# Kernel tuning notes

Measured on AMD Instinct MI355X. Metric: run time of the kernel, lower is better.

The kernel has to match this reference:

```python
import jax, jax.numpy as jnp
import numpy as np

B, S, IN, H, NH, PF, L = 8, 1024, 256, 1024, 16, 4096, 6
HD = H // NH
EPS = 1e-5


def _layernorm(x, g, b):
    m = jnp.mean(x, axis=-1, keepdims=True)
    v = jnp.mean((x - m) ** 2, axis=-1, keepdims=True)
    return (x - m) * jax.lax.rsqrt(v + EPS) * g + b


def setup_inputs() -> dict:
    key = jax.random.key(0)
    ks = iter(jax.random.split(key, 40))
    sd = 0.02
    inp = {
        "input_x": jax.random.normal(next(ks), (B, S, IN), jnp.float32),
        "emb_W": jax.random.normal(next(ks), (IN, H), jnp.float32) * sd,
        "emb_b": jnp.zeros((H,), jnp.float32),
        "pos_tab": jax.random.normal(next(ks), (S, H), jnp.float32) * sd,
        "Wq": jax.random.normal(next(ks), (L, H, H), jnp.float32) * sd,
        "bq": jnp.zeros((L, H), jnp.float32),
        "Wk": jax.random.normal(next(ks), (L, H, H), jnp.float32) * sd,
        "bk": jnp.zeros((L, H), jnp.float32),
        "Wv": jax.random.normal(next(ks), (L, H, H), jnp.float32) * sd,
        "bv": jnp.zeros((L, H), jnp.float32),
        "Wo": jax.random.normal(next(ks), (L, H, H), jnp.float32) * sd,
        "bo": jnp.zeros((L, H), jnp.float32),
        "ln1_g": jnp.ones((L, H), jnp.float32),
        "ln1_b": jnp.zeros((L, H), jnp.float32),
        "W1": jax.random.normal(next(ks), (L, H, PF), jnp.float32) * sd,
        "b1": jnp.zeros((L, PF), jnp.float32),
        "W2": jax.random.normal(next(ks), (L, PF, H), jnp.float32) * sd,
        "b2": jnp.zeros((L, H), jnp.float32),
        "ln2_g": jnp.ones((L, H), jnp.float32),
        "ln2_b": jnp.zeros((L, H), jnp.float32),
    }
    return inp


def _encoder(input_x, emb_W, emb_b, pos_tab, Wq, bq, Wk, bk, Wv, bv, Wo, bo,
             ln1_g, ln1_b, W1, b1, W2, b2, ln2_g, ln2_b):
    scale = jnp.sqrt(jnp.float32(H))  # module scales by sqrt(hidden_size)
    x = (input_x @ emb_W + emb_b) * scale + pos_tab[None, :, :]  # [B,S,H]

    def layer(x, p):
        wq, bq_, wk, bk_, wv, bv_, wo, bo_, g1, be1, w1, b1_, w2, b2_, g2, be2 = p
        q = (x @ wq + bq_).reshape(B, S, NH, HD).transpose(0, 2, 1, 3)  # bhsd
        k = (x @ wk + bk_).reshape(B, S, NH, HD).transpose(0, 2, 1, 3)
        v = (x @ wv + bv_).reshape(B, S, NH, HD).transpose(0, 2, 1, 3)
        energy = jnp.einsum("bhqd,bhkd->bhqk", q, k) / scale  # NOTE: /sqrt(H)
        attn = jax.nn.softmax(energy, axis=-1)
        o = jnp.einsum("bhqk,bhkd->bhqd", attn, v)
        o = o.transpose(0, 2, 1, 3).reshape(B, S, H) @ wo + bo_
        x = _layernorm(x + o, g1, be1)
        f = jax.nn.relu(x @ w1 + b1_) @ w2 + b2_
        x = _layernorm(x + f, g2, be2)
        return x, None

    params = (Wq, bq, Wk, bk, Wv, bv, Wo, bo, ln1_g, ln1_b, W1, b1, W2, b2, ln2_g, ln2_b)
    x, _ = jax.lax.scan(layer, x, params)
    return x


def reference(input_x, emb_W, emb_b, pos_tab, Wq, bq, Wk, bk, Wv, bv, Wo, bo,
              ln1_g, ln1_b, W1, b1, W2, b2, ln2_g, ln2_b):
    return _encoder(input_x, emb_W, emb_b, pos_tab, Wq, bq, Wk, bk, Wv, bv,
                    Wo, bo, ln1_g, ln1_b, W1, b1, W2, b2, ln2_g, ln2_b)
```

## Files before the change

kernel.cpp:

```cpp
#include <hip/hip_runtime.h>

#define HDIM 1024
#define BB 8
#define SS 1024
#define NHEAD 16
#define PFF 4096
#define NLAYER 6
#define MM (BB*SS)

typedef __attribute__((ext_vector_type(8))) short bf16x8_t;
typedef __attribute__((ext_vector_type(4))) float f32x4_t;
typedef __attribute__((ext_vector_type(16))) float f32x16_t;

static __device__ __forceinline__ unsigned short f2b(float f) {
  unsigned int u = __float_as_uint(f);
  u += 0x7fffu + ((u >> 16) & 1u);
  return (unsigned short)(u >> 16);
}

static __device__ __forceinline__ float b2f(unsigned short u) {
  return __uint_as_float(((unsigned)u) << 16);
}

static __device__ __forceinline__ unsigned pkbf(float lo, float hi) {
  unsigned r;
  asm("v_cvt_pk_bf16_f32 %0, %1, %2" : "=v"(r) : "v"(lo), "v"(hi));
  return r;
}

static __device__ __forceinline__ bf16x8_t mk8(unsigned a, unsigned b, unsigned c, unsigned d) {
  union { unsigned u[4]; bf16x8_t v; } x;
  x.u[0] = a; x.u[1] = b; x.u[2] = c; x.u[3] = d;
  return x.v;
}

static __device__ __forceinline__ void gload16(const void* g, void* l) {
  __builtin_amdgcn_global_load_lds((__attribute__((address_space(1))) void*)g,
                                   (__attribute__((address_space(3))) void*)l, 16, 0, 0);
}

template<int N>
static __device__ __forceinline__ void vwait() {
  asm volatile("s_waitcnt vmcnt(%0)" :: "n"(N) : "memory");
}

static __device__ __forceinline__ void bar() {
  asm volatile("" ::: "memory");
  __builtin_amdgcn_s_barrier();
  asm volatile("" ::: "memory");
}

__global__ __launch_bounds__(256) void cvt_bf16(const float* __restrict__ in,
                                                unsigned short* __restrict__ o, int n4) {
  const int i = blockIdx.x * 256 + threadIdx.x;
  if (i < n4) {
    const float4 v = ((const float4*)in)[i];
    ushort4 ob = { f2b(v.x), f2b(v.y), f2b(v.z), f2b(v.w) };
    ((ushort4*)o)[i] = ob;
  }
}

__global__ __launch_bounds__(256) void transpose_bf16(const float* __restrict__ in,
                                                      unsigned short* __restrict__ outT,
                                                      int R, int C) {
  __shared__ float tile[32][33];
  const int c0 = blockIdx.x * 32, r0 = blockIdx.y * 32;
  const int tx = threadIdx.x, ty = threadIdx.y;
#pragma unroll
  for (int i = 0; i < 4; ++i)
    tile[ty + 8*i][tx] = in[(size_t)(r0 + ty + 8*i) * C + c0 + tx];
  __syncthreads();
#pragma unroll
  for (int i = 0; i < 4; ++i)
    outT[(size_t)(c0 + ty + 8*i) * R + r0 + tx] = f2b(tile[tx][ty + 8*i]);
}

__global__ __launch_bounds__(256) void vtrans(const unsigned short* __restrict__ qkv,
                                              unsigned short* __restrict__ vt) {
  __shared__ unsigned short tile[32][34];
  const int s0 = blockIdx.x * 32;
  const int by = blockIdx.y;
  const int bh = by >> 1, dt = by & 1;
  const int b = bh >> 4, h = bh & 15;
  const int tx = threadIdx.x, ty = threadIdx.y;
  const unsigned short* src = qkv + ((size_t)(b * 1024 + s0)) * 3072 + 2048 + h * 64 + dt * 32;
#pragma unroll
  for (int i = 0; i < 4; ++i)
    tile[ty + 8*i][tx] = src[(size_t)(ty + 8*i) * 3072 + tx];
  __syncthreads();
  unsigned short* dst = vt + (size_t)(bh * 64 + dt * 32) * 1024 + s0;
#pragma unroll
  for (int i = 0; i < 4; ++i)
    dst[(size_t)(ty + 8*i) * 1024 + tx] = tile[tx][ty + 8*i];
}

__global__ __launch_bounds__(256) void concat_bias(const float* __restrict__ bq,
                                                   const float* __restrict__ bk,
                                                   const float* __restrict__ bv,
                                                   float* __restrict__ o) {
  const int i = blockIdx.x * 256 + threadIdx.x;
  o[i] = (i < 1024) ? bq[i] : ((i < 2048) ? bk[i - 1024] : bv[i - 2048]);
}

template<int BN, bool BIAS, bool RELU, bool RESID, bool EMB, bool WF32, bool WBF16>
__global__ __launch_bounds__(512, 2) void gemm2c(
    const unsigned short* __restrict__ A,
    const unsigned short* __restrict__ Bt,
    const float* __restrict__ bias,
    const float* __restrict__ resid,
    const float* __restrict__ pos,
    float* __restrict__ outf,
    unsigned short* __restrict__ outb,
    int M, int N, int K) {
  constexpr int NJ = BN / 64;
  constexpr int WCN = BN / 4;
  constexpr int BUFSZ = 32768 + BN * 128;
  __shared__ __align__(1024) char smem[2 * BUFSZ];
  const int t = threadIdx.x, lane = t & 63, w = t >> 6;
  const int wr = w >> 2, wc = w & 3;

  int flat = blockIdx.x + gridDim.x * blockIdx.y;
  const int cpx = (gridDim.x * gridDim.y) >> 3;
  flat = (flat & 7) * cpx + (flat >> 3);
  const int m0 = (flat / gridDim.x) * 256;
  const int n0 = (flat % gridDim.x) * BN;

  const f32x4_t z = {0.f, 0.f, 0.f, 0.f};
  f32x4_t acc[8][NJ];
#pragma unroll
  for (int i = 0; i < 8; ++i)
#pragma unroll
    for (int j = 0; j < NJ; ++j) acc[i][j] = z;

  auto stageA = [&](int i, int kt, int buf) {
    const int chunk = i * 8 + w;
    const int byteoff = chunk * 1024 + lane * 16;
    const int row = byteoff >> 7;
    const int scb = (byteoff & 127) ^ ((row & 7) << 4);
    gload16((const char*)A + ((size_t)(m0 + row) * K + (kt << 6)) * 2 + scb,
            smem + buf * BUFSZ + chunk * 1024);
  };
  auto stageB = [&](int i, int kt, int buf) {
    const int chunk = i * 8 + w;
    const int byteoff = chunk * 1024 + lane * 16;
    const int row = byteoff >> 7;
    const int scb = (byteoff & 127) ^ ((row & 7) << 4);
    gload16((const char*)Bt + ((size_t)(n0 + row) * K + (kt << 6)) * 2 + scb,
            smem + buf * BUFSZ + 32768 + chunk * 1024);
  };
  auto readA = [&](const char* ab, int fi, int ks) {
    const int row = wr * 128 + fi * 16 + (lane & 15);
    const int cb = ks * 64 + ((lane >> 4) << 4);
    return *(const bf16x8_t*)(ab + row * 128 + (cb ^ ((row & 7) << 4)));
  };
  auto readB = [&](const char* bb, int j, int ks) {
    const int row = wc * WCN + j * 16 + (lane & 15);
    const int cb = ks * 64 + ((lane >> 4) << 4);
    return *(const bf16x8_t*)(bb + row * 128 + (cb ^ ((row & 7) << 4)));
  };

  stageB(0, 0, 0); stageB(1, 0, 0);
  if constexpr (NJ >= 3) stageB(2, 0, 0);
  if constexpr (NJ >= 4) stageB(3, 0, 0);
  stageA(0, 0, 0); stageA(2, 0, 0); stageA(1, 0, 0); stageA(3, 0, 0);

  const int nkt = K >> 6;
  for (int kt = 0; kt < nkt; ++kt) {
    const char* ab = smem + (kt & 1) * BUFSZ;
    const char* bb = ab + 32768;
    const int nb = (kt & 1) ^ 1;
    const bool pf = (kt + 1 < nkt);
    bf16x8_t bfr[NJ][2], af[8][2];

    if constexpr (BN >= 192) {
      vwait<2>(); bar();
      if (pf) { stageB(0, kt + 1, nb); stageB(1, kt + 1, nb); }
#pragma unroll
      for (int j = 0; j < NJ; ++j)
#pragma unroll
        for (int ks = 0; ks < 2; ++ks) bfr[j][ks] = readB(bb, j, ks);
#pragma unroll
      for (int d = 0; d < 4; ++d)
#pragma unroll
        for (int ks = 0; ks < 2; ++ks) af[d][ks] = readA(ab, d, ks);
      __builtin_amdgcn_s_setprio(1);
#pragma unroll
      for (int ks = 0; ks < 2; ++ks)
#pragma unroll
        for (int d = 0; d < 2; ++d)
#pragma unroll
          for (int j = 0; j < NJ; ++j)
            acc[d][j] = __builtin_amdgcn_mfma_f32_16x16x32_bf16(af[d][ks], bfr[j][ks], acc[d][j], 0, 0, 0);
      __builtin_amdgcn_s_setprio(0);
      if (pf) vwait<2>(); else vwait<0>();
      bar();
      if (pf) {
        stageB(2, kt + 1, nb);
        if constexpr (NJ >= 4) stageB(3, kt + 1, nb);
        stageA(0, kt + 1, nb);
      }
#pragma unroll
      for (int d = 4; d < 6; ++d)
#pragma unroll
        for (int ks = 0; ks < 2; ++ks) af[d][ks] = readA(ab, d, ks);
      __builtin_amdgcn_s_setprio(1);
#pragma unroll
      for (int ks = 0; ks < 2; ++ks)
#pragma unroll
        for (int d = 2; d < 4; ++d)
#pragma unroll
          for (int j = 0; j < NJ; ++j)
            acc[d][j] = __builtin_amdgcn_mfma_f32_16x16x32_bf16(af[d][ks], bfr[j][ks], acc[d][j], 0, 0, 0);
      __builtin_amdgcn_s_setprio(0);
      if (pf) stageA(2, kt + 1, nb);
#pragma unroll
      for (int d = 6; d < 8; ++d)
#pragma unroll
        for (int ks = 0; ks < 2; ++ks) af[d][ks] = readA(ab, d, ks);
      __builtin_amdgcn_s_setprio(1);
#pragma unroll
      for (int ks = 0; ks < 2; ++ks)
#pragma unroll
        for (int d = 4; d < 6; ++d)
#pragma unroll
          for (int j = 0; j < NJ; ++j)
            acc[d][j] = __builtin_amdgcn_mfma_f32_16x16x32_bf16(af[d][ks], bfr[j][ks], acc[d][j], 0, 0, 0);
      __builtin_amdgcn_s_setprio(0);
      if (pf) { stageA(1, kt + 1, nb); stageA(3, kt + 1, nb); }
      __builtin_amdgcn_s_setprio(1);
#pragma unroll
      for (int ks = 0; ks < 2; ++ks)
#pragma unroll
        for (int d = 6; d < 8; ++d)
#pragma unroll
          for (int j = 0; j < NJ; ++j)
            acc[d][j] = __builtin_amdgcn_mfma_f32_16x16x32_bf16(af[d][ks], bfr[j][ks], acc[d][j], 0, 0, 0);
      __builtin_amdgcn_s_setprio(0);
    } else {
      vwait<2>(); bar();
      if (pf) { stageB(0, kt + 1, nb); stageB(1, kt + 1, nb); stageA(0, kt + 1, nb); }
#pragma unroll
      for (int j = 0; j < NJ; ++j)
#pragma unroll
        for (int ks = 0; ks < 2; ++ks) bfr[j][ks] = readB(bb, j, ks);
#pragma unroll
      for (int d = 0; d < 4; ++d)
#pragma unroll
        for (int ks = 0; ks < 2; ++ks) af[d][ks] = readA(ab, d, ks);
      __builtin_amdgcn_s_setprio(1);
#pragma unroll
      for (int ks = 0; ks < 2; ++ks)
#pragma unroll
        for (int d = 0; d < 4; ++d)
#pragma unroll
          for (int j = 0; j < NJ; ++j)
            acc[d][j] = __builtin_amdgcn_mfma_f32_16x16x32_bf16(af[d][ks], bfr[j][ks], acc[d][j], 0, 0, 0);
      __builtin_amdgcn_s_setprio(0);
      if (pf) vwait<3>(); else vwait<0>();
      bar();
      if (pf) { stageA(2, kt + 1, nb); stageA(1, kt + 1, nb); stageA(3, kt + 1, nb); }
#pragma unroll
      for (int d = 4; d < 8; ++d)
#pragma unroll
        for (int ks = 0; ks < 2; ++ks) af[d][ks] = readA(ab, d, ks);
      __builtin_amdgcn_s_setprio(1);
#pragma unroll
      for (int ks = 0; ks < 2; ++ks)
#pragma unroll
        for (int d = 4; d < 8; ++d)
#pragma unroll
          for (int j = 0; j < NJ; ++j)
            acc[d][j] = __builtin_amdgcn_mfma_f32_16x16x32_bf16(af[d][ks], bfr[j][ks], acc[d][j], 0, 0, 0);
      __builtin_amdgcn_s_setprio(0);
    }
  }

#pragma unroll
  for (int i = 0; i < 8; ++i) {
    const int rbase = m0 + wr * 128 + i * 16 + ((lane >> 4) << 2);
#pragma unroll
    for (int j = 0; j < NJ; ++j) {
      const int cc = n0 + wc * WCN + j * 16 + (lane & 15);
      float bv = 0.f;
      if (BIAS) bv = bias[cc];
#pragma unroll
      for (int r = 0; r < 4; ++r) {
        const int row = rbase + r;
        float v = acc[i][j][r] + bv;
        if (EMB)  v = v * 32.f + pos[(size_t)(row & (SS - 1)) * N + cc];
        if (RELU) v = fmaxf(v, 0.f);
        if (RESID) v += resid[(size_t)row * N + cc];
        if (WF32)  outf[(size_t)row * N + cc] = v;
        if (WBF16) outb[(size_t)row * N + cc] = f2b(v);
      }
    }
  }
}

__global__ __launch_bounds__(256) void attn2(
    const unsigned short* __restrict__ qkv,
    const unsigned short* __restrict__ vt,
    unsigned short* __restrict__ O) {
  __shared__ __align__(1024) char smem[2 * 16384];
  const int t = threadIdx.x, lane = t & 63, w = t >> 6;
  const int l31 = lane & 31, lg = lane >> 5;
  const int bh = blockIdx.y;
  const int b = bh >> 4, h = bh & 15;
  const size_t rowb = (size_t)b << 10;
  const int q0 = blockIdx.x * 128 + w * 32;

  bf16x8_t qf[4];
  {
    const unsigned short* Qp = qkv + (rowb + q0 + l31) * 3072 + h * 64 + lg * 8;
#pragma unroll
    for (int dd = 0; dd < 4; ++dd) qf[dd] = *(const bf16x8_t*)(Qp + dd * 16);
  }

  f32x16_t oa0, oa1;
#pragma unroll
  for (int r = 0; r < 16; ++r) { oa0[r] = 0.f; oa1[r] = 0.f; }
  float m_run = -1e30f, l_run = 0.f;
  const float inv32 = 1.f / 32.f;

  const char* kglob = (const char*)qkv + ((size_t)1024 + h * 64) * 2;
  const char* vglob = (const char*)vt + (size_t)bh * 64 * 1024 * 2;

  auto stage = [&](int kt, int buf) {
    char* kbuf = smem + buf * 16384;
    char* vbuf = kbuf + 8192;
#pragma unroll
    for (int i = 0; i < 2; ++i) {
      const int chunk = w * 2 + i;
      const int byteoff = chunk * 1024 + lane * 16;
      const int row = byteoff >> 7;
      const int scb = (byteoff & 127) ^ ((row & 7) << 4);
      gload16(kglob + (size_t)(rowb + kt * 64 + row) * 6144 + scb, kbuf + chunk * 1024);
      gload16(vglob + ((size_t)row * 1024 + kt * 64) * 2 + scb,    vbuf + chunk * 1024);
    }
  };

  stage(0, 0);
  for (int kt = 0; kt < 16; ++kt) {
    const int cb = kt & 1;
    __syncthreads();
    if (kt < 15) stage(kt + 1, cb ^ 1);
    const char* kbuf = smem + cb * 16384;
    const char* vbuf = kbuf + 8192;

    f32x16_t p0, p1;
#pragma unroll
    for (int r = 0; r < 16; ++r) { p0[r] = 0.f; p1[r] = 0.f; }
    __builtin_amdgcn_s_setprio(1);
#pragma unroll
    for (int dd = 0; dd < 4; ++dd) {
      {
        const int row = l31;
        const int col = (dd * 32 + (lg << 4)) ^ ((row & 7) << 4);
        bf16x8_t kf = *(const bf16x8_t*)(kbuf + row * 128 + col);
        p0 = __builtin_amdgcn_mfma_f32_32x32x16_bf16(kf, qf[dd], p0, 0, 0, 0);
      }
      {
        const int row = 32 + l31;
        const int col = (dd * 32 + (lg << 4)) ^ ((row & 7) << 4);
        bf16x8_t kf = *(const bf16x8_t*)(kbuf + row * 128 + col);
        p1 = __builtin_amdgcn_mfma_f32_32x32x16_bf16(kf, qf[dd], p1, 0, 0, 0);
      }
    }
    __builtin_amdgcn_s_setprio(0);

    float mx = p0[0];
#pragma unroll
    for (int r = 1; r < 16; ++r) mx = fmaxf(mx, p0[r]);
#pragma unroll
    for (int r = 0; r < 16; ++r) mx = fmaxf(mx, p1[r]);
    mx = fmaxf(mx, __shfl_xor(mx, 32));
    const float mn = fmaxf(m_run, mx * inv32);
    const float fr = __expf(m_run - mn);
    m_run = mn;
    float sum = 0.f;
#pragma unroll
    for (int r = 0; r < 16; ++r) { const float e = __expf(p0[r] * inv32 - mn); p0[r] = e; sum += e; }
#pragma unroll
    for (int r = 0; r < 16; ++r) { const float e = __expf(p1[r] * inv32 - mn); p1[r] = e; sum += e; }
    sum += __shfl_xor(sum, 32);
    l_run = l_run * fr + sum;
#pragma unroll
    for (int r = 0; r < 16; ++r) { oa0[r] *= fr; oa1[r] *= fr; }

    const unsigned A0 = pkbf(p0[0], p0[1]),  B0 = pkbf(p0[2], p0[3]);
    const unsigned C0 = pkbf(p0[4], p0[5]),  D0 = pkbf(p0[6], p0[7]);
    const unsigned E0 = pkbf(p0[8], p0[9]),  F0 = pkbf(p0[10], p0[11]);
    const unsigned G0 = pkbf(p0[12], p0[13]), H0 = pkbf(p0[14], p0[15]);
    const unsigned A1 = pkbf(p1[0], p1[1]),  B1 = pkbf(p1[2], p1[3]);
    const unsigned C1 = pkbf(p1[4], p1[5]),  D1 = pkbf(p1[6], p1[7]);
    const unsigned E1 = pkbf(p1[8], p1[9]),  F1 = pkbf(p1[10], p1[11]);
    const unsigned G1 = pkbf(p1[12], p1[13]), H1 = pkbf(p1[14], p1[15]);
    const unsigned sA0 = __shfl_xor((int)A0, 32), sB0 = __shfl_xor((int)B0, 32);
    const unsigned sC0 = __shfl_xor((int)C0, 32), sD0 = __shfl_xor((int)D0, 32);
    const unsigned sE0 = __shfl_xor((int)E0, 32), sF0 = __shfl_xor((int)F0, 32);
    const unsigned sG0 = __shfl_xor((int)G0, 32), sH0 = __shfl_xor((int)H0, 32);
    const unsigned sA1 = __shfl_xor((int)A1, 32), sB1 = __shfl_xor((int)B1, 32);
    const unsigned sC1 = __shfl_xor((int)C1, 32), sD1 = __shfl_xor((int)D1, 32);
    const unsigned sE1 = __shfl_xor((int)E1, 32), sF1 = __shfl_xor((int)F1, 32);
    const unsigned sG1 = __shfl_xor((int)G1, 32), sH1 = __shfl_xor((int)H1, 32);
    const bool hi = (lg != 0);
    bf16x8_t pf[4];
    pf[0] = hi ? mk8(sC0, sD0, C0, D0) : mk8(A0, B0, sA0, sB0);
    pf[1] = hi ? mk8(sG0, sH0, G0, H0) : mk8(E0, F0, sE0, sF0);
    pf[2] = hi ? mk8(sC1, sD1, C1, D1) : mk8(A1, B1, sA1, sB1);
    pf[3] = hi ? mk8(sG1, sH1, G1, H1) : mk8(E1, F1, sE1, sF1);

    __builtin_amdgcn_s_setprio(1);
#pragma unroll
    for (int c = 0; c < 4; ++c) {
      {
        const int row = l31;
        const int col = (c * 32 + (lg << 4)) ^ ((row & 7) << 4);
        bf16x8_t vf = *(const bf16x8_t*)(vbuf + row * 128 + col);
        oa0 = __builtin_amdgcn_mfma_f32_32x32x16_bf16(vf, pf[c], oa0, 0, 0, 0);
      }
      {
        const int row = 32 + l31;
        const int col = (c * 32 + (lg << 4)) ^ ((row & 7) << 4);
        bf16x8_t vf = *(const bf16x8_t*)(vbuf + row * 128 + col);
        oa1 = __builtin_amdgcn_mfma_f32_32x32x16_bf16(vf, pf[c], oa1, 0, 0, 0);
      }
    }
    __builtin_amdgcn_s_setprio(0);
  }

  const float inv = 1.f / l_run;
  unsigned short* op = O + (rowb + q0 + l31) * 1024 + h * 64 + (lg << 2);
#pragma unroll
  for (int rg = 0; rg < 4; ++rg) {
    const unsigned u0 = pkbf(oa0[rg * 4 + 0] * inv, oa0[rg * 4 + 1] * inv);
    const unsigned u1 = pkbf(oa0[rg * 4 + 2] * inv, oa0[rg * 4 + 3] * inv);
    uint2 st = { u0, u1 };
    *(uint2*)(op + rg * 8) = st;
    const unsigned v0 = pkbf(oa1[rg * 4 + 0] * inv, oa1[rg * 4 + 1] * inv);
    const unsigned v1 = pkbf(oa1[rg * 4 + 2] * inv, oa1[rg * 4 + 3] * inv);
    uint2 st2 = { v0, v1 };
    *(uint2*)(op + 32 + rg * 8) = st2;
  }
}

__global__ __launch_bounds__(256) void lnb_kernel(
    const unsigned short* __restrict__ yb, const float* __restrict__ g,
    const float* __restrict__ be,
    float* __restrict__ xf, unsigned short* __restrict__ xb) {
  const int row = blockIdx.x;
  const int t = threadIdx.x;
  const ushort4 u = ((const ushort4*)(yb + (size_t)row * HDIM))[t];
  float4 v = { b2f(u.x), b2f(u.y), b2f(u.z), b2f(u.w) };
  float s  = v.x + v.y + v.z + v.w;
  float ss = v.x*v.x + v.y*v.y + v.z*v.z + v.w*v.w;
#pragma unroll
  for (int m = 1; m < 64; m <<= 1) { s += __shfl_xor(s, m); ss += __shfl_xor(ss, m); }
  __shared__ float rs[4], rss[4];
  const int w = t >> 6, lane = t & 63;
  if (lane == 0) { rs[w] = s; rss[w] = ss; }
  __syncthreads();
  s  = rs[0] + rs[1] + rs[2] + rs[3];
  ss = rss[0] + rss[1] + rss[2] + rss[3];
  const float mean = s * (1.f / HDIM);
  const float inv = rsqrtf(ss * (1.f / HDIM) - mean * mean + 1e-5f);
  const int c = t * 4;
  const float4 gg = *(const float4*)(g + c);
  const float4 bb = *(const float4*)(be + c);
  float4 o;
  o.x = (v.x - mean) * inv * gg.x + bb.x;
  o.y = (v.y - mean) * inv * gg.y + bb.y;
  o.z = (v.z - mean) * inv * gg.z + bb.z;
  o.w = (v.w - mean) * inv * gg.w + bb.w;
  ((float4*)(xf + (size_t)row * HDIM))[t] = o;
  ushort4 ob = { f2b(o.x), f2b(o.y), f2b(o.z), f2b(o.w) };
  ((ushort4*)(xb + (size_t)row * HDIM))[t] = ob;
}

extern "C" void kernel_launch(void* const* d_in, const int* in_sizes, int n_in,
                              void* d_out, int out_size, void* d_ws, size_t ws_size,
                              hipStream_t stream) {
  const float* input_x = (const float*)d_in[0];
  const float* emb_W   = (const float*)d_in[1];
  const float* emb_b   = (const float*)d_in[2];
  const float* pos_tab = (const float*)d_in[3];
  const float* Wq  = (const float*)d_in[4];
  const float* bq  = (const float*)d_in[5];
  const float* Wk  = (const float*)d_in[6];
  const float* bk  = (const float*)d_in[7];
  const float* Wv  = (const float*)d_in[8];
  const float* bv  = (const float*)d_in[9];
  const float* Wo  = (const float*)d_in[10];
  const float* bo  = (const float*)d_in[11];
  const float* ln1g = (const float*)d_in[12];
  const float* ln1b = (const float*)d_in[13];
  const float* W1  = (const float*)d_in[14];
  const float* b1  = (const float*)d_in[15];
  const float* W2  = (const float*)d_in[16];
  const float* b2  = (const float*)d_in[17];
  const float* ln2g = (const float*)d_in[18];
  const float* ln2b = (const float*)d_in[19];
  float* out = (float*)d_out;

  char* ws = (char*)d_ws;
  size_t off = 0;
  auto alloc = [&](size_t bytes) {
    char* p = ws + off;
    off += (bytes + 255) & ~(size_t)255;
    return p;
  };
  unsigned short* wqkvT = (unsigned short*)alloc((size_t)3072 * HDIM * 2);
  unsigned short* woT   = (unsigned short*)alloc((size_t)HDIM * HDIM * 2);
  unsigned short* w1T   = (unsigned short*)alloc((size_t)PFF * HDIM * 2);
  unsigned short* w2T   = (unsigned short*)alloc((size_t)HDIM * PFF * 2);
  unsigned short* embWT = (unsigned short*)alloc((size_t)HDIM * 256 * 2);
  float*          bqkv  = (float*)alloc(3072 * 4);
  unsigned short* inb   = (unsigned short*)alloc((size_t)MM * 256 * 2);
  unsigned short* xb    = (unsigned short*)alloc((size_t)MM * HDIM * 2);
  unsigned short* qkvb  = (unsigned short*)alloc((size_t)MM * 3072 * 2);
  unsigned short* vtb   = (unsigned short*)alloc((size_t)MM * HDIM * 2);
  unsigned short* ab    = (unsigned short*)alloc((size_t)MM * HDIM * 2);
  unsigned short* yb    = (unsigned short*)alloc((size_t)MM * HDIM * 2);
  unsigned short* hb = qkvb;

  const dim3 blk256(256);
  const dim3 blk512(512);
  const dim3 tblk(32, 8);

  cvt_bf16<<<dim3(MM * 256 / 4 / 256), blk256, 0, stream>>>(input_x, inb, MM * 256 / 4);
  transpose_bf16<<<dim3(HDIM / 32, 256 / 32), tblk, 0, stream>>>(emb_W, embWT, 256, HDIM);

  gemm2c<128, true, false, false, true, true, true><<<dim3(HDIM / 128, MM / 256), blk512, 0, stream>>>(
      inb, embWT, emb_b, nullptr, pos_tab, out, xb, MM, HDIM, 256);

  for (int l = 0; l < NLAYER; ++l) {
    const size_t wofs = (size_t)l * HDIM * HDIM;
    transpose_bf16<<<dim3(32, 32), tblk, 0, stream>>>(Wq + wofs, wqkvT,               HDIM, HDIM);
    transpose_bf16<<<dim3(32, 32), tblk, 0, stream>>>(Wk + wofs, wqkvT + 1024 * 1024, HDIM, HDIM);
    transpose_bf16<<<dim3(32, 32), tblk, 0, stream>>>(Wv + wofs, wqkvT + 2048 * 1024, HDIM, HDIM);
    transpose_bf16<<<dim3(32, 32), tblk, 0, stream>>>(Wo + wofs, woT, HDIM, HDIM);
    transpose_bf16<<<dim3(PFF / 32, HDIM / 32), tblk, 0, stream>>>(
        W1 + (size_t)l * HDIM * PFF, w1T, HDIM, PFF);
    transpose_bf16<<<dim3(HDIM / 32, PFF / 32), tblk, 0, stream>>>(
        W2 + (size_t)l * PFF * HDIM, w2T, PFF, HDIM);
    concat_bias<<<dim3(12), blk256, 0, stream>>>(bq + l * HDIM, bk + l * HDIM, bv + l * HDIM, bqkv);

    gemm2c<192, true, false, false, false, false, true><<<dim3(3072 / 192, MM / 256), blk512, 0, stream>>>(
        xb, wqkvT, bqkv, nullptr, nullptr, nullptr, qkvb, MM, 3072, HDIM);

    vtrans<<<dim3(32, 256), tblk, 0, stream>>>(qkvb, vtb);

    attn2<<<dim3(SS / 128, BB * NHEAD), blk256, 0, stream>>>(qkvb, vtb, ab);

    gemm2c<128, true, false, true, false, false, true><<<dim3(HDIM / 128, MM / 256), blk512, 0, stream>>>(
        ab, woT, bo + l * HDIM, out, nullptr, nullptr, yb, MM, HDIM, HDIM);
    lnb_kernel<<<dim3(MM), blk256, 0, stream>>>(yb, ln1g + l * HDIM, ln1b + l * HDIM, out, xb);

    gemm2c<256, true, true, false, false, false, true><<<dim3(PFF / 256, MM / 256), blk512, 0, stream>>>(
        xb, w1T, b1 + (size_t)l * PFF, nullptr, nullptr, nullptr, hb, MM, PFF, HDIM);
    gemm2c<128, true, false, true, false, false, true><<<dim3(HDIM / 128, MM / 256), blk512, 0, stream>>>(
        hb, w2T, b2 + l * HDIM, out, nullptr, nullptr, yb, MM, HDIM, PFF);
    lnb_kernel<<<dim3(MM), blk256, 0, stream>>>(yb, ln2g + l * HDIM, ln2b + l * HDIM, out, xb);
  }
  (void)in_sizes; (void)n_in; (void)out_size; (void)ws_size;
}
```

Baseline: 2.222 ms.

## Fuse per-layer weight transposes into one kernel and write V transposed from QKV GEMM

The six per-layer weight-transpose launches and the bias concat are merged into one prep_layer kernel that dispatches on block index. The QKV GEMM epilogue now writes the V columns directly in the transposed [b,h,d,s] layout the attention kernel reads, which removes the separate vtrans kernel and its extra pass over V. The cost is fewer launches and less memory traffic per layer. In exchange, V stores from the epilogue are packed 8-byte writes strided by the sequence length, and the prep kernel adds branching.

```diff
diff --git a/kernel.cpp b/kernel.cpp
--- a/kernel.cpp
+++ b/kernel.cpp
@@ -75,34 +75,42 @@
     outT[(size_t)(c0 + ty + 8*i) * R + r0 + tx] = f2b(tile[tx][ty + 8*i]);
 }
 
-__global__ __launch_bounds__(256) void vtrans(const unsigned short* __restrict__ qkv,
-                                              unsigned short* __restrict__ vt) {
-  __shared__ unsigned short tile[32][34];
-  const int s0 = blockIdx.x * 32;
-  const int by = blockIdx.y;
-  const int bh = by >> 1, dt = by & 1;
-  const int b = bh >> 4, h = bh & 15;
+__global__ __launch_bounds__(256) void prep_layer(
+    const float* __restrict__ Wq, const float* __restrict__ Wk,
+    const float* __restrict__ Wv, const float* __restrict__ Wo,
+    const float* __restrict__ W1, const float* __restrict__ W2,
+    const float* __restrict__ bq, const float* __restrict__ bk,
+    const float* __restrict__ bv,
+    unsigned short* __restrict__ wqkvT, unsigned short* __restrict__ woT,
+    unsigned short* __restrict__ w1T, unsigned short* __restrict__ w2T,
+    float* __restrict__ bqkv) {
+  const int id = blockIdx.x;
   const int tx = threadIdx.x, ty = threadIdx.y;
-  const unsigned short* src = qkv + ((size_t)(b * 1024 + s0)) * 3072 + 2048 + h * 64 + dt * 32;
+  if (id >= 12288) {
+    const int i = (id - 12288) * 256 + ty * 32 + tx;
+    bqkv[i] = (i < 1024) ? bq[i] : ((i < 2048) ? bk[i - 1024] : bv[i - 2048]);
+    return;
+  }
+  __shared__ float tile[32][33];
+  const float* in; unsigned short* outp; int R, C, tid;
+  if (id < 1024)      { in = Wq; outp = wqkvT;           R = 1024; C = 1024; tid = id; }
+  else if (id < 2048) { in = Wk; outp = wqkvT + 1048576; R = 1024; C = 1024; tid = id - 1024; }
+  else if (id < 3072) { in = Wv; outp = wqkvT + 2097152; R = 1024; C = 1024; tid = id - 2048; }
+  else if (id < 4096) { in = Wo; outp = woT;             R = 1024; C = 1024; tid = id - 3072; }
+  else if (id < 8192) { in = W1; outp = w1T;             R = 1024; C = 4096; tid = id - 4096; }
+  else                { in = W2; outp = w2T;             R = 4096; C = 1024; tid = id - 8192; }
+  const int gxn = C >> 5;
+  const int c0 = (tid % gxn) * 32, r0 = (tid / gxn) * 32;
 #pragma unroll
   for (int i = 0; i < 4; ++i)
-    tile[ty + 8*i][tx] = src[(size_t)(ty + 8*i) * 3072 + tx];
+    tile[ty + 8*i][tx] = in[(size_t)(r0 + ty + 8*i) * C + c0 + tx];
   __syncthreads();
-  unsigned short* dst = vt + (size_t)(bh * 64 + dt * 32) * 1024 + s0;
 #pragma unroll
   for (int i = 0; i < 4; ++i)
-    dst[(size_t)(ty + 8*i) * 1024 + tx] = tile[tx][ty + 8*i];
-}
-
-__global__ __launch_bounds__(256) void concat_bias(const float* __restrict__ bq,
-                                                   const float* __restrict__ bk,
-                                                   const float* __restrict__ bv,
-                                                   float* __restrict__ o) {
-  const int i = blockIdx.x * 256 + threadIdx.x;
-  o[i] = (i < 1024) ? bq[i] : ((i < 2048) ? bk[i - 1024] : bv[i - 2048]);
-}
-
-template<int BN, bool BIAS, bool RELU, bool RESID, bool EMB, bool WF32, bool WBF16>
+    outp[(size_t)(c0 + ty + 8*i) * R + r0 + tx] = f2b(tile[tx][ty + 8*i]);
+}
+
+template<int BN, bool BIAS, bool RELU, bool RESID, bool EMB, bool WF32, bool WBF16, bool VTW>
 __global__ __launch_bounds__(512, 2) void gemm2c(
     const unsigned short* __restrict__ A,
     const unsigned short* __restrict__ Bt,
@@ -111,6 +119,7 @@
     const float* __restrict__ pos,
     float* __restrict__ outf,
     unsigned short* __restrict__ outb,
+    unsigned short* __restrict__ vtw,
     int M, int N, int K) {
   constexpr int NJ = BN / 64;
   constexpr int WCN = BN / 4;
@@ -283,15 +292,27 @@
       const int cc = n0 + wc * WCN + j * 16 + (lane & 15);
       float bv = 0.f;
       if (BIAS) bv = bias[cc];
-#pragma unroll
-      for (int r = 0; r < 4; ++r) {
-        const int row = rbase + r;
-        float v = acc[i][j][r] + bv;
-        if (EMB)  v = v * 32.f + pos[(size_t)(row & (SS - 1)) * N + cc];
-        if (RELU) v = fmaxf(v, 0.f);
-        if (RESID) v += resid[(size_t)row * N + cc];
-        if (WF32)  outf[(size_t)row * N + cc] = v;
-        if (WBF16) outb[(size_t)row * N + cc] = f2b(v);
+      bool vpath = false;
+      if constexpr (VTW) vpath = (cc >= 2048);
+      if (vpath) {
+        const float v0 = acc[i][j][0] + bv, v1 = acc[i][j][1] + bv;
+        const float v2 = acc[i][j][2] + bv, v3 = acc[i][j][3] + bv;
+        const int d = cc - 2048;
+        const int b = rbase >> 10, s = rbase & 1023;
+        unsigned short* vp = vtw + ((size_t)(((b << 4) | (d >> 6)) << 6 | (d & 63))) * 1024 + s;
+        uint2 st = { pkbf(v0, v1), pkbf(v2, v3) };
+        *(uint2*)vp = st;
+      } else {
+#pragma unroll
+        for (int r = 0; r < 4; ++r) {
+          const int row = rbase + r;
+          float v = acc[i][j][r] + bv;
+          if (EMB)  v = v * 32.f + pos[(size_t)(row & (SS - 1)) * N + cc];
+          if (RELU) v = fmaxf(v, 0.f);
+          if (RESID) v += resid[(size_t)row * N + cc];
+          if (WF32)  outf[(size_t)row * N + cc] = v;
+          if (WBF16) outb[(size_t)row * N + cc] = f2b(v);
+        }
       }
     }
   }
@@ -530,36 +551,30 @@
   cvt_bf16<<<dim3(MM * 256 / 4 / 256), blk256, 0, stream>>>(input_x, inb, MM * 256 / 4);
   transpose_bf16<<<dim3(HDIM / 32, 256 / 32), tblk, 0, stream>>>(emb_W, embWT, 256, HDIM);
 
-  gemm2c<128, true, false, false, true, true, true><<<dim3(HDIM / 128, MM / 256), blk512, 0, stream>>>(
-      inb, embWT, emb_b, nullptr, pos_tab, out, xb, MM, HDIM, 256);
+  gemm2c<128, true, false, false, true, true, true, false><<<dim3(HDIM / 128, MM / 256), blk512, 0, stream>>>(
+      inb, embWT, emb_b, nullptr, pos_tab, out, xb, nullptr, MM, HDIM, 256);
 
   for (int l = 0; l < NLAYER; ++l) {
     const size_t wofs = (size_t)l * HDIM * HDIM;
-    transpose_bf16<<<dim3(32, 32), tblk, 0, stream>>>(Wq + wofs, wqkvT,               HDIM, HDIM);
-    transpose_bf16<<<dim3(32, 32), tblk, 0, stream>>>(Wk + wofs, wqkvT + 1024 * 1024, HDIM, HDIM);
-    transpose_bf16<<<dim3(32, 32), tblk, 0, stream>>>(Wv + wofs, wqkvT + 2048 * 1024, HDIM, HDIM);
-    transpose_bf16<<<dim3(32, 32), tblk, 0, stream>>>(Wo + wofs, woT, HDIM, HDIM);
-    transpose_bf16<<<dim3(PFF / 32, HDIM / 32), tblk, 0, stream>>>(
-        W1 + (size_t)l * HDIM * PFF, w1T, HDIM, PFF);
-    transpose_bf16<<<dim3(HDIM / 32, PFF / 32), tblk, 0, stream>>>(
-        W2 + (size_t)l * PFF * HDIM, w2T, PFF, HDIM);
-    concat_bias<<<dim3(12), blk256, 0, stream>>>(bq + l * HDIM, bk + l * HDIM, bv + l * HDIM, bqkv);
-
-    gemm2c<192, true, false, false, false, false, true><<<dim3(3072 / 192, MM / 256), blk512, 0, stream>>>(
-        xb, wqkvT, bqkv, nullptr, nullptr, nullptr, qkvb, MM, 3072, HDIM);
-
-    vtrans<<<dim3(32, 256), tblk, 0, stream>>>(qkvb, vtb);
+    prep_layer<<<dim3(12300), tblk, 0, stream>>>(
+        Wq + wofs, Wk + wofs, Wv + wofs, Wo + wofs,
+        W1 + (size_t)l * HDIM * PFF, W2 + (size_t)l * PFF * HDIM,
+        bq + l * HDIM, bk + l * HDIM, bv + l * HDIM,
+        wqkvT, woT, w1T, w2T, bqkv);
+
+    gemm2c<192, true, false, false, false, false, true, true><<<dim3(3072 / 192, MM / 256), blk512, 0, stream>>>(
+        xb, wqkvT, bqkv, nullptr, nullptr, nullptr, qkvb, vtb, MM, 3072, HDIM);
 
     attn2<<<dim3(SS / 128, BB * NHEAD), blk256, 0, stream>>>(qkvb, vtb, ab);
 
-    gemm2c<128, true, false, true, false, false, true><<<dim3(HDIM / 128, MM / 256), blk512, 0, stream>>>(
-        ab, woT, bo + l * HDIM, out, nullptr, nullptr, yb, MM, HDIM, HDIM);
+    gemm2c<128, true, false, true, false, false, true, false><<<dim3(HDIM / 128, MM / 256), blk512, 0, stream>>>(
+        ab, woT, bo + l * HDIM, out, nullptr, nullptr, yb, nullptr, MM, HDIM, HDIM);
     lnb_kernel<<<dim3(MM), blk256, 0, stream>>>(yb, ln1g + l * HDIM, ln1b + l * HDIM, out, xb);
 
-    gemm2c<256, true, true, false, false, false, true><<<dim3(PFF / 256, MM / 256), blk512, 0, stream>>>(
-        xb, w1T, b1 + (size_t)l * PFF, nullptr, nullptr, nullptr, hb, MM, PFF, HDIM);
-    gemm2c<128, true, false, true, false, false, true><<<dim3(HDIM / 128, MM / 256), blk512, 0, stream>>>(
-        hb, w2T, b2 + l * HDIM, out, nullptr, nullptr, yb, MM, HDIM, PFF);
+    gemm2c<256, true, true, false, false, false, true, false><<<dim3(PFF / 256, MM / 256), blk512, 0, stream>>>(
+        xb, w1T, b1 + (size_t)l * PFF, nullptr, nullptr, nullptr, hb, nullptr, MM, PFF, HDIM);
+    gemm2c<128, true, false, true, false, false, true, false><<<dim3(HDIM / 128, MM / 256), blk512, 0, stream>>>(
+        hb, w2T, b2 + l * HDIM, out, nullptr, nullptr, yb, nullptr, MM, HDIM, PFF);
     lnb_kernel<<<dim3(MM), blk256, 0, stream>>>(yb, ln2g + l * HDIM, ln2b + l * HDIM, out, xb);
   }
   (void)in_sizes; (void)n_in; (void)out_size; (void)ws_size;
```

After: 2.139 ms. 3.7% less time.
